# Optimization experiments

Measured on AMD Instinct MI355X. Metric: run time of the kernel, lower is better.

## Reference

```python
import jax, jax.numpy as jnp
import numpy as np

N_HEAD = 16


def setup_inputs() -> dict:
    key = jax.random.key(0)
    ks = jax.random.split(key, 9)
    b, s, d = 4, 2048, 1024
    scale = 1.0 / np.sqrt(d)
    return {
        "x": jax.random.normal(ks[0], (b, s, d), dtype=jnp.float32),
        "Wq": jax.random.normal(ks[1], (d, d), dtype=jnp.float32) * scale,
        "bq": jax.random.normal(ks[2], (d,), dtype=jnp.float32) * 0.01,
        "Wk": jax.random.normal(ks[3], (d, d), dtype=jnp.float32) * scale,
        "bk": jax.random.normal(ks[4], (d,), dtype=jnp.float32) * 0.01,
        "Wv": jax.random.normal(ks[5], (d, d), dtype=jnp.float32) * scale,
        "bv": jax.random.normal(ks[6], (d,), dtype=jnp.float32) * 0.01,
        "Wo": jax.random.normal(ks[7], (d, d), dtype=jnp.float32) * scale,
        "bo": jax.random.normal(ks[8], (d,), dtype=jnp.float32) * 0.01,
        "mask": 1,
    }


def reference(x, Wq, bq, Wk, bk, Wv, bv, Wo, bo, mask):
    b, s, d = x.shape
    h = N_HEAD
    dh = d // h
    # projections -> [b, h, s, dh]
    def proj(W, bias):
        return (x @ W + bias).reshape(b, s, h, dh).transpose(0, 2, 1, 3)

    Q = proj(Wq, bq)
    K = proj(Wk, bk)
    V = proj(Wv, bv)

    # full S x S scores (module materializes them explicitly)
    scores = jnp.einsum('bhqd,bhkd->bhqk', Q, K)
    if mask:
        causal = jnp.triu(jnp.ones((s, s), dtype=bool), k=1)
        scores = jnp.where(causal, -jnp.inf, scores)
    scores = scores / jnp.sqrt(jnp.asarray(dh, dtype=scores.dtype))
    attn = jax.nn.softmax(scores, axis=-1)
    out = jnp.einsum('bhqk,bhkd->bhqd', attn, V)  # [b, h, s, dh]
    out = out.transpose(0, 2, 1, 3).reshape(b, s, d)
    return out @ Wo + bo
```

## Files before the change

### kernel.cpp

```cpp
#include <hip/hip_runtime.h>

typedef unsigned short u16;
typedef unsigned int u32;
typedef __bf16 bf16x8 __attribute__((ext_vector_type(8)));
typedef float f32x4 __attribute__((ext_vector_type(4)));

#define BATCH 4
#define SLEN 2048
#define DMODEL 1024
#define NHEAD 16
#define DHEAD 64
#define MROWS (BATCH * SLEN)

__device__ __forceinline__ u16 f32_to_bf16(float f) {
  u32 u = __float_as_uint(f);
  u32 r = (u + 0x7FFFu + ((u >> 16) & 1u)) >> 16;
  return (u16)r;
}
__device__ __forceinline__ u32 pack_bf16x2(float a, float b) {
  return (u32)f32_to_bf16(a) | ((u32)f32_to_bf16(b) << 16);
}

__device__ __forceinline__ u32 pack_trunc(float lo, float hi) {
#if __has_builtin(__builtin_amdgcn_perm)
  return __builtin_amdgcn_perm(__float_as_uint(hi), __float_as_uint(lo), 0x07060302u);
#else
  return (__float_as_uint(hi) & 0xFFFF0000u) | (__float_as_uint(lo) >> 16);
#endif
}
__device__ __forceinline__ u32 pack_round(float lo, float hi) {
  u32 ul = __float_as_uint(lo) + 0x8000u;
  u32 uh = __float_as_uint(hi) + 0x8000u;
#if __has_builtin(__builtin_amdgcn_perm)
  return __builtin_amdgcn_perm(uh, ul, 0x07060302u);
#else
  return (uh & 0xFFFF0000u) | (ul >> 16);
#endif
}

#if __has_builtin(__builtin_amdgcn_exp2f)
#define EXP2(x) __builtin_amdgcn_exp2f(x)
#else
#define EXP2(x) exp2f(x)
#endif

typedef const __attribute__((address_space(1))) void* gas_cv;
typedef __attribute__((address_space(3))) void* las_v;
__device__ __forceinline__ void async16(const u16* g, u16* l) {
  __builtin_amdgcn_global_load_lds((gas_cv)g, (las_v)l, 16, 0, 0);
}


__global__ void convert_x_kernel(const float* __restrict__ x, u16* __restrict__ xb) {
  size_t i = ((size_t)blockIdx.x * 256 + threadIdx.x) * 8;
  float4 v0 = *(const float4*)(x + i);
  float4 v1 = *(const float4*)(x + i + 4);
  uint4 o;
  o.x = pack_bf16x2(v0.x, v0.y);
  o.y = pack_bf16x2(v0.z, v0.w);
  o.z = pack_bf16x2(v1.x, v1.y);
  o.w = pack_bf16x2(v1.z, v1.w);
  *(uint4*)(xb + i) = o;
}

__global__ void transpose_w_kernel(const float* __restrict__ Wq, const float* __restrict__ Wk,
                                   const float* __restrict__ Wv, const float* __restrict__ Wo,
                                   u16* __restrict__ wqkvt, u16* __restrict__ wot) {
  __shared__ float tile[32][33];
  int z = blockIdx.z;
  const float* src = (z == 0) ? Wq : (z == 1) ? Wk : (z == 2) ? Wv : Wo;
  u16* dst = (z < 3) ? (wqkvt + (size_t)z * DMODEL * DMODEL) : wot;
  int c0 = blockIdx.x * 32, r0 = blockIdx.y * 32;
  int tx = threadIdx.x & 31, ty = threadIdx.x >> 5;
#pragma unroll
  for (int i = 0; i < 4; ++i)
    tile[ty + 8 * i][tx] = src[(size_t)(r0 + ty + 8 * i) * DMODEL + c0 + tx];
  __syncthreads();
#pragma unroll
  for (int i = 0; i < 4; ++i)
    dst[(size_t)(c0 + ty + 8 * i) * DMODEL + r0 + tx] = f32_to_bf16(tile[tx][ty + 8 * i]);
}

__global__ void concat_bias_kernel(const float* __restrict__ bq, const float* __restrict__ bk,
                                   const float* __restrict__ bv, float* __restrict__ bqkv) {
  int i = blockIdx.x * 256 + threadIdx.x;
  float v = (i < 1024) ? bq[i] : (i < 2048) ? bk[i - 1024] : bv[i - 2048];
  bqkv[i] = v;
}

__global__ void transpose_v_kernel(const u16* __restrict__ qkv, u16* __restrict__ vt) {
  __shared__ u16 tile[32][33];
  const int bh = blockIdx.z;
  const int b = bh >> 4, h = bh & 15;
  const int s0 = blockIdx.x * 32, d0 = blockIdx.y * 32;
  const int tx = threadIdx.x & 31, ty = threadIdx.x >> 5;
#pragma unroll
  for (int i = 0; i < 4; ++i)
    tile[ty + 8 * i][tx] =
        qkv[(size_t)(b * SLEN + s0 + ty + 8 * i) * (3 * DMODEL) + 2 * DMODEL + h * DHEAD + d0 + tx];
  __syncthreads();
#pragma unroll
  for (int i = 0; i < 4; ++i)
    vt[(size_t)(bh * DHEAD + d0 + ty + 8 * i) * SLEN + s0 + tx] = tile[tx][ty + 8 * i];
}

template <int OUT_BF16>
__global__ __launch_bounds__(256) void gemm_bt_kernel(const u16* __restrict__ A,
                                                      const u16* __restrict__ Bt,
                                                      const float* __restrict__ bias,
                                                      void* __restrict__ Cout,
                                                      int M, int N, int K) {
  __shared__ u16 sA[128 * 32];
  __shared__ u16 sB[128 * 32];
  const int tid = threadIdx.x;
  const int wv = tid >> 6, lane = tid & 63;
  const int wr = wv >> 1, wc = wv & 1;
  const int col = lane & 15, quad = lane >> 4;
  const int m0 = blockIdx.x * 128;
  const int n0 = blockIdx.y * 128;

  f32x4 acc[4][4] = {};

  const int lr = tid >> 2;
  const int ls = tid & 3;
  const size_t a_base = (size_t)(m0 + lr) * K + ls * 8;
  const size_t b_base = (size_t)(n0 + lr) * K + ls * 8;
  u16* ldsA0 = sA + ((tid >> 6) << 9);
  u16* ldsA1 = ldsA0 + 2048;
  u16* ldsB0 = sB + ((tid >> 6) << 9);
  u16* ldsB1 = ldsB0 + 2048;

  for (int k0 = 0; k0 < K; k0 += 32) {
    async16(A + a_base + k0, ldsA0);
    async16(A + a_base + (size_t)64 * K + k0, ldsA1);
    async16(Bt + b_base + k0, ldsB0);
    async16(Bt + b_base + (size_t)64 * K + k0, ldsB1);
    __syncthreads();
    bf16x8 af[4], bfr[4];
#pragma unroll
    for (int i = 0; i < 4; ++i)
      af[i] = *(const bf16x8*)(sA + (wr * 64 + i * 16 + col) * 32 + quad * 8);
#pragma unroll
    for (int j = 0; j < 4; ++j)
      bfr[j] = *(const bf16x8*)(sB + (wc * 64 + j * 16 + col) * 32 + quad * 8);
#pragma unroll
    for (int i = 0; i < 4; ++i)
#pragma unroll
      for (int j = 0; j < 4; ++j)
        acc[i][j] = __builtin_amdgcn_mfma_f32_16x16x32_bf16(af[i], bfr[j], acc[i][j], 0, 0, 0);
    __syncthreads();
  }

#pragma unroll
  for (int i = 0; i < 4; ++i) {
#pragma unroll
    for (int j = 0; j < 4; ++j) {
      int n = n0 + wc * 64 + j * 16 + col;
      float bia = bias[n];
#pragma unroll
      for (int r = 0; r < 4; ++r) {
        int m = m0 + wr * 64 + i * 16 + quad * 4 + r;
        float v = acc[i][j][r] + bia;
        if (OUT_BF16)
          ((u16*)Cout)[(size_t)m * N + n] = f32_to_bf16(v);
        else
          ((float*)Cout)[(size_t)m * N + n] = v;
      }
    }
  }
}

__global__ __launch_bounds__(256, 4) void attn_kernel(const u16* __restrict__ qkv,
                                                      const u16* __restrict__ vt,
                                                      u16* __restrict__ out) {
  const int bh = blockIdx.y;
  const int b = bh >> 4, h = bh & 15;
  const int tid = threadIdx.x;
  const int wv = tid >> 6, lane = tid & 63;
  const int col = lane & 15, quad = lane >> 4;
  const int bx = blockIdx.x;
  const int sfirst = bx * 4 + wv;

  __shared__ u16 sK[2][64 * 64];
  __shared__ u16 sV[2][64 * 64];
  __shared__ u16 sP[4][16 * 64];
  u16* mysP = sP[wv];

  const u16* kbase = qkv + ((size_t)(b * SLEN)) * (3 * DMODEL) + DMODEL + h * DHEAD;
  const u16* vbase = vt + ((size_t)bh * DHEAD) * SLEN;
  const float scl2 = 0.125f * 1.44269504088896f;

  const int lrow = lane >> 3;
  const int sga = (lane & 7) ^ lrow;
  const int r0a = wv * 16, r0b = wv * 16 + 8;

  for (int half = 0; half < 2; ++half) {
    const int s2 = half ? (127 - sfirst) : sfirst;
    const int qbase = s2 * 16;
    const int nt = half ? (32 - bx) : (bx + 1);

    const u16* qrow = qkv + ((size_t)(b * SLEN + qbase + col)) * (3 * DMODEL) + h * DHEAD;
    bf16x8 aQ[2];
#pragma unroll
    for (int ks = 0; ks < 2; ++ks)
      aQ[ks] = *(const bf16x8*)(qrow + ks * 32 + quad * 8);

    f32x4 accO[4] = {};
    float m2 = -1e30f, l_i = 0.0f;

    async16(kbase + (size_t)(r0a + lrow) * (3 * DMODEL) + sga * 8, sK[0] + r0a * 64);
    async16(kbase + (size_t)(r0b + lrow) * (3 * DMODEL) + sga * 8, sK[0] + r0b * 64);
    async16(vbase + (size_t)(r0a + lrow) * SLEN + sga * 8, sV[0] + r0a * 64);
    async16(vbase + (size_t)(r0b + lrow) * SLEN + sga * 8, sV[0] + r0b * 64);
    __syncthreads();

    for (int t = 0; t < nt; ++t) {
      const int kv0 = t * 64;
      const int cur = t & 1, nxt = cur ^ 1;

      if (t + 1 < nt) {
        const int kvn = kv0 + 64;
        async16(kbase + (size_t)(kvn + r0a + lrow) * (3 * DMODEL) + sga * 8, sK[nxt] + r0a * 64);
        async16(kbase + (size_t)(kvn + r0b + lrow) * (3 * DMODEL) + sga * 8, sK[nxt] + r0b * 64);
        async16(vbase + (size_t)(r0a + lrow) * SLEN + kvn + sga * 8, sV[nxt] + r0a * 64);
        async16(vbase + (size_t)(r0b + lrow) * SLEN + kvn + sga * 8, sV[nxt] + r0b * 64);
      }

      const u16* sKc = sK[cur];
      const u16* sVc = sV[cur];
      bf16x8 bK[2][4], bV[2][4];
#pragma unroll
      for (int ks = 0; ks < 2; ++ks) {
        const int sl = (((ks * 4 + quad) ^ (col & 7)) * 8);
#pragma unroll
        for (int cb = 0; cb < 4; ++cb)
          bK[ks][cb] = *(const bf16x8*)(sKc + (cb * 16 + col) * 64 + sl);
#pragma unroll
        for (int j = 0; j < 4; ++j)
          bV[ks][j] = *(const bf16x8*)(sVc + (j * 16 + col) * 64 + sl);
      }

      f32x4 accST[4] = {};
#pragma unroll
      for (int ks = 0; ks < 2; ++ks)
#pragma unroll
        for (int cb = 0; cb < 4; ++cb)
          accST[cb] = __builtin_amdgcn_mfma_f32_16x16x32_bf16(bK[ks][cb], aQ[ks],
                                                              accST[cb], 0, 0, 0);

      if (t == nt - 1) {
        int q = qbase + col;
#pragma unroll
        for (int cb = 0; cb < 4; ++cb) {
          int kvb = kv0 + cb * 16 + quad * 4;
#pragma unroll
          for (int r = 0; r < 4; ++r)
            if (kvb + r > q) accST[cb][r] = -1e30f;
        }
      }

      float rmax = accST[0][0];
#pragma unroll
      for (int cb = 0; cb < 4; ++cb)
#pragma unroll
        for (int r = 0; r < 4; ++r) rmax = fmaxf(rmax, accST[cb][r]);
      rmax = fmaxf(rmax, __shfl_xor(rmax, 16));
      rmax = fmaxf(rmax, __shfl_xor(rmax, 32));
      float mnew = fmaxf(m2, rmax * scl2);
      float alpha = EXP2(m2 - mnew);
      m2 = mnew;
      float sacc = 0.0f;
#pragma unroll
      for (int cb = 0; cb < 4; ++cb)
#pragma unroll
        for (int r = 0; r < 4; ++r) {
          float p = EXP2(__builtin_fmaf(accST[cb][r], scl2, -mnew));
          accST[cb][r] = p;
          sacc += p;
        }
      sacc += __shfl_xor(sacc, 16);
      sacc += __shfl_xor(sacc, 32);
      l_i = l_i * alpha + sacc;
#pragma unroll
      for (int j = 0; j < 4; ++j)
#pragma unroll
        for (int r = 0; r < 4; ++r) accO[j][r] *= alpha;

#pragma unroll
      for (int cb = 0; cb < 4; ++cb) {
        uint2 pk;
        pk.x = pack_trunc(accST[cb][0], accST[cb][1]);
        pk.y = pack_trunc(accST[cb][2], accST[cb][3]);
        *(uint2*)(mysP + col * 64 + (((cb * 2 + (quad >> 1)) ^ (col & 7)) << 3) +
                  ((quad & 1) << 2)) = pk;
      }
      bf16x8 aP[2];
#pragma unroll
      for (int ks = 0; ks < 2; ++ks)
        aP[ks] = *(const bf16x8*)(mysP + col * 64 + (((ks * 4 + quad) ^ (col & 7)) << 3));

#pragma unroll
      for (int ks = 0; ks < 2; ++ks)
#pragma unroll
        for (int j = 0; j < 4; ++j)
          accO[j] = __builtin_amdgcn_mfma_f32_16x16x32_bf16(bV[ks][j], aP[ks],
                                                            accO[j], 0, 0, 0);

      __syncthreads();
    }

    {
      float rl = 1.0f / l_i;
      size_t rowoff = ((size_t)(b * SLEN + qbase + col)) * DMODEL + h * DHEAD;
#pragma unroll
      for (int j = 0; j < 4; ++j) {
        uint2 pk;
        pk.x = pack_round(accO[j][0] * rl, accO[j][1] * rl);
        pk.y = pack_round(accO[j][2] * rl, accO[j][3] * rl);
        *(uint2*)(out + rowoff + j * 16 + quad * 4) = pk;
      }
    }
  }
}


extern "C" void kernel_launch(void* const* d_in, const int* in_sizes, int n_in,
                              void* d_out, int out_size, void* d_ws, size_t ws_size,
                              hipStream_t stream) {
  const float* x = (const float*)d_in[0];
  const float* Wq = (const float*)d_in[1];
  const float* bq = (const float*)d_in[2];
  const float* Wk = (const float*)d_in[3];
  const float* bk = (const float*)d_in[4];
  const float* Wv = (const float*)d_in[5];
  const float* bv = (const float*)d_in[6];
  const float* Wo = (const float*)d_in[7];
  const float* bo = (const float*)d_in[8];

  char* ws = (char*)d_ws;
  u16* xb = (u16*)ws;
  u16* wqkvt = (u16*)(ws + ((size_t)16 << 20));
  u16* wot = (u16*)(ws + ((size_t)22 << 20));
  u16* qkv = (u16*)(ws + ((size_t)24 << 20));
  u16* attnO = (u16*)(ws + ((size_t)72 << 20));
  float* bqkv = (float*)(ws + ((size_t)88 << 20));
  u16* vtp = xb;

  convert_x_kernel<<<4096, 256, 0, stream>>>(x, xb);
  transpose_w_kernel<<<dim3(32, 32, 4), 256, 0, stream>>>(Wq, Wk, Wv, Wo, wqkvt, wot);
  concat_bias_kernel<<<12, 256, 0, stream>>>(bq, bk, bv, bqkv);
  gemm_bt_kernel<1><<<dim3(64, 24), 256, 0, stream>>>(xb, wqkvt, bqkv, (void*)qkv,
                                                      MROWS, 3 * DMODEL, DMODEL);
  transpose_v_kernel<<<dim3(64, 2, 64), 256, 0, stream>>>(qkv, vtp);
  attn_kernel<<<dim3(16, BATCH * NHEAD), 256, 0, stream>>>(qkv, vtp, attnO);
  gemm_bt_kernel<0><<<dim3(64, 8), 256, 0, stream>>>(attnO, wot, bo, d_out,
                                                     MROWS, DMODEL, DMODEL);
}
```

Baseline: 299.2 us.

## Load K fragments directly from global and skip softmax rescale when max unchanged

K tiles now go straight from global memory into MFMA operand registers instead of being staged through double-buffered LDS. This removes the sK buffers and their LDS writes and reads, but each wave now issues its own uncoalesced global loads with no prefetch overlap. The online softmax also skips the rescale of the accumulator and row sum when no lane's new max exceeds the running max, checked wave-wide with __all. The row max is computed as a balanced tree instead of a serial chain.

Measured after the change: 354.0 us. 18.3% more time.

```diff
diff --git a/kernel.cpp b/kernel.cpp
--- a/kernel.cpp
+++ b/kernel.cpp
@@ -181,7 +181,6 @@
   const int bx = blockIdx.x;
   const int sfirst = bx * 4 + wv;
 
-  __shared__ u16 sK[2][64 * 64];
   __shared__ u16 sV[2][64 * 64];
   __shared__ u16 sP[4][16 * 64];
   u16* mysP = sP[wv];
@@ -193,6 +192,8 @@
   const int lrow = lane >> 3;
   const int sga = (lane & 7) ^ lrow;
   const int r0a = wv * 16, r0b = wv * 16 + 8;
+
+  const u16* kfrag = kbase + (size_t)col * (3 * DMODEL) + quad * 8;
 
   for (int half = 0; half < 2; ++half) {
     const int s2 = half ? (127 - sfirst) : sfirst;
@@ -208,8 +209,6 @@
     f32x4 accO[4] = {};
     float m2 = -1e30f, l_i = 0.0f;
 
-    async16(kbase + (size_t)(r0a + lrow) * (3 * DMODEL) + sga * 8, sK[0] + r0a * 64);
-    async16(kbase + (size_t)(r0b + lrow) * (3 * DMODEL) + sga * 8, sK[0] + r0b * 64);
     async16(vbase + (size_t)(r0a + lrow) * SLEN + sga * 8, sV[0] + r0a * 64);
     async16(vbase + (size_t)(r0b + lrow) * SLEN + sga * 8, sV[0] + r0b * 64);
     __syncthreads();
@@ -218,23 +217,27 @@
       const int kv0 = t * 64;
       const int cur = t & 1, nxt = cur ^ 1;
 
+      bf16x8 bK[2][4];
+      {
+        const u16* kt = kfrag + (size_t)kv0 * (3 * DMODEL);
+#pragma unroll
+        for (int ks = 0; ks < 2; ++ks)
+#pragma unroll
+          for (int cb = 0; cb < 4; ++cb)
+            bK[ks][cb] = *(const bf16x8*)(kt + (size_t)(cb * 16) * (3 * DMODEL) + ks * 32);
+      }
+
       if (t + 1 < nt) {
         const int kvn = kv0 + 64;
-        async16(kbase + (size_t)(kvn + r0a + lrow) * (3 * DMODEL) + sga * 8, sK[nxt] + r0a * 64);
-        async16(kbase + (size_t)(kvn + r0b + lrow) * (3 * DMODEL) + sga * 8, sK[nxt] + r0b * 64);
         async16(vbase + (size_t)(r0a + lrow) * SLEN + kvn + sga * 8, sV[nxt] + r0a * 64);
         async16(vbase + (size_t)(r0b + lrow) * SLEN + kvn + sga * 8, sV[nxt] + r0b * 64);
       }
 
-      const u16* sKc = sK[cur];
       const u16* sVc = sV[cur];
-      bf16x8 bK[2][4], bV[2][4];
+      bf16x8 bV[2][4];
 #pragma unroll
       for (int ks = 0; ks < 2; ++ks) {
         const int sl = (((ks * 4 + quad) ^ (col & 7)) * 8);
-#pragma unroll
-        for (int cb = 0; cb < 4; ++cb)
-          bK[ks][cb] = *(const bf16x8*)(sKc + (cb * 16 + col) * 64 + sl);
 #pragma unroll
         for (int j = 0; j < 4; ++j)
           bV[ks][j] = *(const bf16x8*)(sVc + (j * 16 + col) * 64 + sl);
@@ -259,15 +262,17 @@
         }
       }
 
-      float rmax = accST[0][0];
-#pragma unroll
-      for (int cb = 0; cb < 4; ++cb)
-#pragma unroll
-        for (int r = 0; r < 4; ++r) rmax = fmaxf(rmax, accST[cb][r]);
+      float ma = fmaxf(fmaxf(accST[0][0], accST[0][1]), fmaxf(accST[0][2], accST[0][3]));
+      float mb = fmaxf(fmaxf(accST[1][0], accST[1][1]), fmaxf(accST[1][2], accST[1][3]));
+      float mc = fmaxf(fmaxf(accST[2][0], accST[2][1]), fmaxf(accST[2][2], accST[2][3]));
+      float md = fmaxf(fmaxf(accST[3][0], accST[3][1]), fmaxf(accST[3][2], accST[3][3]));
+      float rmax = fmaxf(fmaxf(ma, mb), fmaxf(mc, md));
       rmax = fmaxf(rmax, __shfl_xor(rmax, 16));
       rmax = fmaxf(rmax, __shfl_xor(rmax, 32));
-      float mnew = fmaxf(m2, rmax * scl2);
-      float alpha = EXP2(m2 - mnew);
+      float rmaxs = rmax * scl2;
+      const bool noresc = __all(rmaxs <= m2);
+      float mnew = noresc ? m2 : fmaxf(m2, rmaxs);
+      float alpha = noresc ? 1.0f : EXP2(m2 - mnew);
       m2 = mnew;
       float sacc = 0.0f;
 #pragma unroll
@@ -280,11 +285,15 @@
         }
       sacc += __shfl_xor(sacc, 16);
       sacc += __shfl_xor(sacc, 32);
-      l_i = l_i * alpha + sacc;
-#pragma unroll
-      for (int j = 0; j < 4; ++j)
-#pragma unroll
-        for (int r = 0; r < 4; ++r) accO[j][r] *= alpha;
+      if (noresc) {
+        l_i += sacc;
+      } else {
+        l_i = l_i * alpha + sacc;
+#pragma unroll
+        for (int j = 0; j < 4; ++j)
+#pragma unroll
+          for (int r = 0; r < 4; ++r) accO[j][r] *= alpha;
+      }
 
 #pragma unroll
       for (int cb = 0; cb < 4; ++cb) {
```
